# Optimization experiments

Measured on AMD Instinct MI355X. Metric: run time of the kernel, lower is better.

Reference implementation:

```python
import jax, jax.numpy as jnp
import numpy as np
from jax import lax

D, H, W = 50, 50, 50
EPS = 1e-5


def _conv_bn_relu(x, k, gamma, beta, stride):
    # x: (B, Cin, D, H, W), k: (Cout, Cin, 3, 3, 3)
    y = lax.conv_general_dilated(
        x, k, window_strides=(stride, stride, stride),
        padding=[(1, 1), (1, 1), (1, 1)],
        dimension_numbers=("NCDHW", "OIDHW", "NCDHW"))
    # BatchNorm3d in training mode: batch statistics over (N, D, H, W)
    mean = jnp.mean(y, axis=(0, 2, 3, 4), keepdims=True)
    var = jnp.var(y, axis=(0, 2, 3, 4), keepdims=True)
    y = (y - mean) * lax.rsqrt(var + EPS)
    y = y * gamma.reshape(1, -1, 1, 1, 1) + beta.reshape(1, -1, 1, 1, 1)
    return jax.nn.relu(y)


def setup_inputs() -> dict:
    key = jax.random.key(0)
    ks = jax.random.split(key, 16)
    B, N, P, C = 4, 8192, 32, 8
    VD = 128
    s = 0.05
    inp = {
        "voxel_features": jax.random.normal(ks[0], (B, N, P, C), jnp.float32),
        "voxel_coords": jax.random.randint(ks[1], (B, N, 3), 0, 50, jnp.int32),
        "W1": jax.random.normal(ks[2], (C, 64), jnp.float32) * s,
        "b1": jnp.zeros((64,), jnp.float32),
        "W2": jax.random.normal(ks[3], (64, 128), jnp.float32) * s,
        "b2": jnp.zeros((128,), jnp.float32),
        "W3": jax.random.normal(ks[4], (128, VD), jnp.float32) * s,
        "b3": jnp.zeros((VD,), jnp.float32),
        "k1": jax.random.normal(ks[5], (64, VD, 3, 3, 3), jnp.float32) * s,
        "g1": jnp.ones((64,), jnp.float32),
        "be1": jnp.zeros((64,), jnp.float32),
        "k2": jax.random.normal(ks[6], (128, 64, 3, 3, 3), jnp.float32) * s,
        "g2": jnp.ones((128,), jnp.float32),
        "be2": jnp.zeros((128,), jnp.float32),
    }
    return inp


def reference(voxel_features, voxel_coords, W1, b1, W2, b2, W3, b3,
              k1, g1, be1, k2, g2, be2):
    B, N, P, C = voxel_features.shape
    # --- VFE: per-point MLP then max-pool over the P points of each voxel ---
    h = jax.nn.relu(voxel_features @ W1 + b1)      # (B, N, P, 64)
    h = jax.nn.relu(h @ W2 + b2)                   # (B, N, P, 128)
    h = h @ W3 + b3                                # (B, N, P, VD)
    feats = jnp.max(h, axis=2)                     # (B, N, VD)  == MaxPool1d(32)
    VD = feats.shape[-1]
    # --- scatter voxel features into dense grid (replaces B*N python loop) ---
    b_idx = jnp.broadcast_to(jnp.arange(B)[:, None], (B, N))
    vx, vy, vz = voxel_coords[..., 0], voxel_coords[..., 1], voxel_coords[..., 2]
    grid = jnp.zeros((B, D, H, W, VD), feats.dtype)
    grid = grid.at[b_idx, vx, vy, vz].set(feats)   # channel-last scatter
    grid = jnp.transpose(grid, (0, 4, 1, 2, 3))    # (B, VD, D, H, W)
    # --- Conv3d + BN + ReLU stack ---
    y = _conv_bn_relu(grid, k1, g1, be1, stride=1)  # (B, 64, 50, 50, 50)
    y = _conv_bn_relu(y, k2, g2, be2, stride=2)     # (B, 128, 25, 25, 25)
    return y
```

## Files before the change

kernel.cpp:

```cpp
#include <hip/hip_runtime.h>

typedef unsigned short u16;
typedef unsigned int u32;
typedef __attribute__((ext_vector_type(8))) short bf16x8;
typedef __attribute__((ext_vector_type(4))) float f32x4;

#define NB 4
#define NVOX 8192
#define GD 50
#define CELLS 125000

#define OWNER_OFF 0u
#define STATS_OFF 2000000u
#define WT1_OFF   2003072u
#define WT2_OFF   2445440u
#define VW2F_OFF  2887808u
#define VW3F_OFF  2904192u
#define FEATS_OFF 2936960u
#define Y1F_OFF   11325568u

#define S1_SUM 0
#define S1_SQ  64
#define SC1    128
#define SH1    192
#define S2_SUM 256
#define S2_SQ  384
#define SC2    512
#define SH2    640

__device__ __forceinline__ float bf2f(u16 v){ union{u32 u; float f;} x; x.u=((u32)v)<<16; return x.f; }
__device__ __forceinline__ u16 f2bf(float f){ union{u32 u; float f;} x; x.f=f; u32 r = x.u + 0x7fffu + ((x.u>>16)&1u); return (u16)(r>>16); }
__device__ __forceinline__ f32x4 fzero(){ f32x4 v; v[0]=0.f; v[1]=0.f; v[2]=0.f; v[3]=0.f; return v; }

__global__ void k_wt_transform(const float* __restrict__ k1, const float* __restrict__ k2,
                               const float* __restrict__ W2, const float* __restrict__ W3,
                               u16* __restrict__ wt1, u16* __restrict__ wt2,
                               u16* __restrict__ vw2f, u16* __restrict__ vw3f) {
    int idx = blockIdx.x * 256 + threadIdx.x;
    if (idx < 221184) {
        {
            int j = idx & 7, co = (idx>>3)&63, kq = (idx>>9)&3, kc = (idx>>11)&3, s = idx>>13;
            int ci = kc*32 + kq*8 + j;
            wt1[idx] = f2bf(k1[(co*128 + ci)*27 + s]);
        }
        {
            int j = idx & 7, co = (idx>>3)&127, kq = (idx>>10)&3, kc = (idx>>12)&1, s = idx>>13;
            int ci = kc*32 + kq*8 + j;
            wt2[idx] = f2bf(k2[(co*64 + ci)*27 + s]);
        }
    }
    if (idx < 8192) {
        int j = idx & 7, n = (idx>>3)&127, q = idx>>10;
        vw2f[idx] = f2bf(W2[(q*8+j)*128 + n]);
    }
    if (idx < 16384) {
        int j = idx & 7, n = (idx>>3)&127, q = idx>>10;
        vw3f[idx] = f2bf(W3[(q*8+j)*128 + n]);
    }
}

__global__ void k_owner(const int* __restrict__ coords, int* __restrict__ owner) {
    int v = blockIdx.x * 256 + threadIdx.x;
    if (v >= NB*NVOX) return;
    int b = v >> 13, n = v & (NVOX-1);
    int x = coords[v*3], y = coords[v*3+1], z = coords[v*3+2];
    atomicMax(&owner[b*CELLS + (x*GD + y)*GD + z], n);
}

__global__ __launch_bounds__(256, 2) void k_vfe(
        const float* __restrict__ vf,
        const float* __restrict__ W1, const float* __restrict__ b1,
        const float* __restrict__ b2, const float* __restrict__ b3,
        const u16* __restrict__ vw2f, const u16* __restrict__ vw3f,
        u16* __restrict__ feats) {
    const int bid = blockIdx.x;
    const int t = threadIdx.x;
    const int w = t >> 6, lane = t & 63;
    const int lo = lane & 15, hi = lane >> 4;
    const int chgrp = w >> 1, pgrp = w & 1;

    __shared__ __align__(16) char pool[49152];
    u16* h1s = (u16*)pool;
    char* h2s = pool + 16384;
    float* red = (float*)(pool + 16384);

    bf16x8 wa2[2][4], wa3[4][4];
    #pragma unroll
    for (int kk = 0; kk < 2; ++kk)
        #pragma unroll
        for (int cf = 0; cf < 4; ++cf)
            wa2[kk][cf] = *(const bf16x8*)(vw2f + (((kk*4+hi)*128) + chgrp*64 + cf*16 + lo)*8);
    #pragma unroll
    for (int kk = 0; kk < 4; ++kk)
        #pragma unroll
        for (int cf = 0; cf < 4; ++cf)
            wa3[kk][cf] = *(const bf16x8*)(vw3f + (((kk*4+hi)*128) + chgrp*64 + cf*16 + lo)*8);
    f32x4 bb2[4];
    #pragma unroll
    for (int cf = 0; cf < 4; ++cf)
        bb2[cf] = *(const f32x4*)(b2 + chgrp*64 + cf*16 + hi*4);

    {
        const int pt = t & 127, C0 = (t >> 7) * 32;
        f32x4 xv0 = *(const f32x4*)(vf + (size_t)(bid*128 + pt)*8);
        f32x4 xv1 = *(const f32x4*)(vf + (size_t)(bid*128 + pt)*8 + 4);
        float x[8] = {xv0[0],xv0[1],xv0[2],xv0[3],xv1[0],xv1[1],xv1[2],xv1[3]};
        float h[32];
        #pragma unroll
        for (int c = 0; c < 32; ++c) h[c] = b1[C0 + c];
        #pragma unroll
        for (int k = 0; k < 8; ++k) {
            float xk = x[k];
            #pragma unroll
            for (int c = 0; c < 32; ++c) h[c] += xk * W1[k*64 + C0 + c];
        }
        #pragma unroll
        for (int c8 = 0; c8 < 4; ++c8) {
            u16 d8[8];
            #pragma unroll
            for (int j = 0; j < 8; ++j) d8[j] = f2bf(fmaxf(h[c8*8 + j], 0.f));
            int slot = ((C0 >> 3) + c8) ^ (pt & 7);
            *(uint4*)(h1s + pt*64 + slot*8) = *(uint4*)d8;
        }
    }
    __syncthreads();

    f32x4 acc2[4][4];
    #pragma unroll
    for (int cf = 0; cf < 4; ++cf)
        #pragma unroll
        for (int pf = 0; pf < 4; ++pf) acc2[cf][pf] = fzero();
    #pragma unroll
    for (int kk = 0; kk < 2; ++kk) {
        bf16x8 bh[4];
        #pragma unroll
        for (int pf = 0; pf < 4; ++pf) {
            int pt = pgrp*64 + pf*16 + lo;
            bh[pf] = *(const bf16x8*)(h1s + pt*64 + (((kk*4+hi) ^ (pt&7)) << 3));
        }
        #pragma unroll
        for (int cf = 0; cf < 4; ++cf)
            #pragma unroll
            for (int pf = 0; pf < 4; ++pf)
                acc2[cf][pf] = __builtin_amdgcn_mfma_f32_16x16x32_bf16(wa2[kk][cf], bh[pf], acc2[cf][pf], 0, 0, 0);
    }
    #pragma unroll
    for (int cf = 0; cf < 4; ++cf) {
        #pragma unroll
        for (int pf = 0; pf < 4; ++pf) {
            int pt = pgrp*64 + pf*16 + lo;
            float v0 = fmaxf(acc2[cf][pf][0] + bb2[cf][0], 0.f);
            float v1 = fmaxf(acc2[cf][pf][1] + bb2[cf][1], 0.f);
            float v2 = fmaxf(acc2[cf][pf][2] + bb2[cf][2], 0.f);
            float v3 = fmaxf(acc2[cf][pf][3] + bb2[cf][3], 0.f);
            uint2 d;
            d.x = (u32)f2bf(v0) | ((u32)f2bf(v1) << 16);
            d.y = (u32)f2bf(v2) | ((u32)f2bf(v3) << 16);
            int s = (chgrp*8 + cf*2 + (hi>>1)) ^ (pt & 15);
            *(uint2*)(h2s + pt*256 + s*16 + (hi&1)*8) = d;
        }
    }
    __syncthreads();

    f32x4 acc3[4][4];
    #pragma unroll
    for (int cf = 0; cf < 4; ++cf)
        #pragma unroll
        for (int pf = 0; pf < 4; ++pf) acc3[cf][pf] = fzero();
    #pragma unroll
    for (int kk = 0; kk < 4; ++kk) {
        bf16x8 bh[4];
        #pragma unroll
        for (int pf = 0; pf < 4; ++pf) {
            int pt = pgrp*64 + pf*16 + lo;
            bh[pf] = *(const bf16x8*)(h2s + pt*256 + (((kk*4+hi) ^ (pt&15)) << 4));
        }
        #pragma unroll
        for (int cf = 0; cf < 4; ++cf)
            #pragma unroll
            for (int pf = 0; pf < 4; ++pf)
                acc3[cf][pf] = __builtin_amdgcn_mfma_f32_16x16x32_bf16(wa3[kk][cf], bh[pf], acc3[cf][pf], 0, 0, 0);
    }
    __syncthreads();

    #pragma unroll
    for (int vox01 = 0; vox01 < 2; ++vox01) {
        int vv = pgrp*2 + vox01;
        #pragma unroll
        for (int cf = 0; cf < 4; ++cf) {
            f32x4 mx;
            #pragma unroll
            for (int r = 0; r < 4; ++r)
                mx[r] = fmaxf(acc3[cf][vox01*2][r], acc3[cf][vox01*2+1][r]);
            int s4 = (cf*4 + hi) ^ lo;
            *(f32x4*)(red + vv*2048 + lo*128 + chgrp*64 + s4*4) = mx;
        }
    }
    __syncthreads();

    #pragma unroll
    for (int half = 0; half < 2; ++half) {
        int vv = (t >> 7) + half*2;
        int ch = t & 127;
        int cq = (ch & 63) >> 2, e = ch & 3, cg = ch >> 6;
        float m = -3.0e38f;
        #pragma unroll
        for (int lo2 = 0; lo2 < 16; ++lo2)
            m = fmaxf(m, red[vv*2048 + lo2*128 + cg*64 + ((cq ^ lo2) << 2) + e]);
        int gv = bid*4 + vv;
        feats[(size_t)gv*128 + ch] = f2bf(m + b3[ch]);
    }
}

__global__ __launch_bounds__(256, 3) void k_conv1t(
        const u16* __restrict__ feats, const int* __restrict__ owner,
        const u16* __restrict__ wt1, float* __restrict__ y1f,
        float* __restrict__ stats) {
    const int tx = blockIdx.x, ty = blockIdx.y;
    const int b = blockIdx.z >> 1, h = blockIdx.z & 1;
    const int z0 = h*25;
    const int t = threadIdx.x;
    const int w = t >> 6, lane = t & 63;
    const int lo = lane & 15, hi = lane >> 4;

    __shared__ __align__(16) float acc[4*100*20];
    __shared__ int list[432];
    __shared__ int cnt;

    if (t == 0) cnt = 0;
    for (int i = t; i < 2000; i += 256)
        *(f32x4*)(acc + i*4) = fzero();
    __syncthreads();

    for (int i = t; i < 432; i += 256) {
        int hxr = i / 108, r2 = i - hxr*108;
        int hyr = r2 / 27, zz = r2 - hyr*27;
        int z = z0 - 1 + zz;
        int hx = 2*tx - 1 + hxr, hy = 2*ty - 1 + hyr;
        if (hx >= 0 && hx < GD && hy >= 0 && hy < GD && z >= 0 && z < GD) {
            int n = owner[b*CELLS + (hx*GD + hy)*GD + z];
            if (n >= 0) {
                int idx = atomicAdd(&cnt, 1);
                list[idx] = n | (hxr << 13) | (hyr << 15) | (z << 17);
            }
        }
    }
    __syncthreads();
    const int C = cnt;
    float* accw = acc + w*2000;

    for (int g = 0; g*32 < C; ++g) {
        int e0 = 0, e1 = 0; bool v0 = false, v1 = false;
        { int i0 = g*32 + lo;      if (i0 < C) { e0 = list[i0]; v0 = true; } }
        { int i1 = g*32 + 16 + lo; if (i1 < C) { e1 = list[i1]; v1 = true; } }
        const u16* f0 = feats + (size_t)(b*NVOX + (e0 & 8191))*128 + hi*8;
        const u16* f1 = feats + (size_t)(b*NVOX + (e1 & 8191))*128 + hi*8;
        bf16x8 bb0[4], bb1[4];
        #pragma unroll
        for (int kc = 0; kc < 4; ++kc) bb0[kc] = *(const bf16x8*)(f0 + kc*32);
        #pragma unroll
        for (int kc = 0; kc < 4; ++kc) bb1[kc] = *(const bf16x8*)(f1 + kc*32);
        const int hx0 = (e0>>13)&3, hy0 = (e0>>15)&3, zz0 = (e0>>17)&63;
        const int hx1 = (e1>>13)&3, hy1 = (e1>>15)&3, zz1 = (e1>>17)&63;
        const bool two = (g*32 + 16 < C);

        #pragma unroll 1
        for (int s = 0; s < 27; ++s) {
            const int dx = s/9, r9 = s - dx*9, dy = r9/3, dz = r9 - dy*3;
            bf16x8 a[4];
            #pragma unroll
            for (int kc = 0; kc < 4; ++kc)
                a[kc] = *(const bf16x8*)(wt1 + (size_t)((s*4 + kc)*4 + hi)*512 + (w*16 + lo)*8);
            {
                int oxr = hx0 - dx, oyr = hy0 - dy, ozl = zz0 + 1 - dz - z0;
                bool val = v0 && ((unsigned)oxr < 2u) && ((unsigned)oyr < 2u)
                              && ((unsigned)ozl < 25u);
                f32x4 d = fzero();
                #pragma unroll
                for (int kc = 0; kc < 4; ++kc)
                    d = __builtin_amdgcn_mfma_f32_16x16x32_bf16(a[kc], bb0[kc], d, 0, 0, 0);
                if (val) {
                    float* p = accw + ((oxr*2 + oyr)*25 + ozl)*20 + hi*4;
                    f32x4 o = *(f32x4*)p;
                    o[0] += d[0]; o[1] += d[1]; o[2] += d[2]; o[3] += d[3];
                    *(f32x4*)p = o;
                }
            }
            if (two) {
                int oxr = hx1 - dx, oyr = hy1 - dy, ozl = zz1 + 1 - dz - z0;
                bool val = v1 && ((unsigned)oxr < 2u) && ((unsigned)oyr < 2u)
                              && ((unsigned)ozl < 25u);
                f32x4 d = fzero();
                #pragma unroll
                for (int kc = 0; kc < 4; ++kc)
                    d = __builtin_amdgcn_mfma_f32_16x16x32_bf16(a[kc], bb1[kc], d, 0, 0, 0);
                if (val) {
                    float* p = accw + ((oxr*2 + oyr)*25 + ozl)*20 + hi*4;
                    f32x4 o = *(f32x4*)p;
                    o[0] += d[0]; o[1] += d[1]; o[2] += d[2]; o[3] += d[3];
                    *(f32x4*)p = o;
                }
            }
        }
    }
    __syncthreads();

    float s4[4] = {0.f,0.f,0.f,0.f}, q4[4] = {0.f,0.f,0.f,0.f};
    const int cq = t & 15;
    for (int i = t; i < 1600; i += 256) {
        int cell = i >> 4;
        f32x4 v = *(const f32x4*)(acc + (cq>>2)*2000 + cell*20 + (cq&3)*4);
        int col = cell / 25, ozl = cell - col*25;
        int ox = 2*tx + (col >> 1), oy = 2*ty + (col & 1);
        *(f32x4*)(y1f + (size_t)((b*GD + ox)*GD + oy)*3200 + (z0 + ozl)*64 + cq*4) = v;
        #pragma unroll
        for (int e2 = 0; e2 < 4; ++e2) { s4[e2] += v[e2]; q4[e2] += v[e2]*v[e2]; }
    }
    __syncthreads();
    #pragma unroll
    for (int e2 = 0; e2 < 4; ++e2) {
        acc[t*8 + e2]     = s4[e2];
        acc[t*8 + 4 + e2] = q4[e2];
    }
    __syncthreads();
    if (t < 128) {
        int isq = t >> 6, ch = t & 63, cq0 = ch >> 2, e2 = ch & 3;
        float sum = 0.f;
        #pragma unroll
        for (int k = 0; k < 16; ++k)
            sum += acc[(cq0 + 16*k)*8 + isq*4 + e2];
        atomicAdd(&stats[(isq ? S1_SQ : S1_SUM) + ch], sum);
    }
}

__global__ void k_finalize(float* __restrict__ stats, const float* __restrict__ g,
                           const float* __restrict__ be, int C, float cnt,
                           int st_off, int sc_off, int sh_off) {
    int t = threadIdx.x;
    if (t < C) {
        float mean = stats[st_off + t] / cnt;
        float var  = stats[st_off + C + t] / cnt - mean*mean;
        float inv  = rsqrtf(var + 1e-5f);
        stats[sc_off + t] = g[t]*inv;
        stats[sh_off + t] = be[t] - mean*g[t]*inv;
    }
}

__global__ __launch_bounds__(256, 4) void k_conv2(
        const float* __restrict__ y1f, const u16* __restrict__ wt2,
        float* __restrict__ stats, float* __restrict__ out) {
    const int ox = blockIdx.x, oyp = blockIdx.y, b = blockIdx.z;
    const int t = threadIdx.x;
    const int w = t >> 6, lane = t & 63;
    const int col = w >> 1, nh = w & 1, lo = lane & 15, hi = lane >> 4;

    __shared__ __align__(16) char pool[26624];
    u16* in2 = (u16*)pool;
    float* red2 = (float*)(pool + 25600);
    red2[t] = 0.f;

    const float* sc1 = stats + SC1;
    const float* sh1 = stats + SH1;

    f32x4 acc[2][4];
    #pragma unroll
    for (int m=0;m<2;m++){ acc[m][0]=fzero(); acc[m][1]=fzero(); acc[m][2]=fzero(); acc[m][3]=fzero(); }

    const int oy = 2*oyp + col;
    for (int dxy = 0; dxy < 9; ++dxy) {
        int dx = dxy/3, dy = dxy - dx*3;
        int xi = 2*ox + dx - 1;
        bool okx = (xi >= 0) && (xi < GD);
        __syncthreads();
        for (int i = t; i < 832; i += 256) {
            int c = (i >= 416) ? 1 : 0;
            int cc = i - c*416;
            int z = cc >> 3, sl = cc & 7;
            int oyc = 2*oyp + c;
            int yi = 2*oyc + dy - 1;
            bool ok = okx && (oyc < 25) && (yi >= 0) && (yi < GD) && (z >= 1) && (z <= 50);
            u16 d8[8];
            if (ok) {
                const float* src = y1f + (size_t)((b*GD + xi)*GD + yi)*3200 + cc*8 - 64;
                f32x4 v0 = *(const f32x4*)src;
                f32x4 v1 = *(const f32x4*)(src + 4);
                #pragma unroll
                for (int j=0;j<4;j++) {
                    int ci = sl*8 + j;
                    d8[j] = f2bf(fmaxf(v0[j]*sc1[ci] + sh1[ci], 0.f));
                }
                #pragma unroll
                for (int j=0;j<4;j++) {
                    int ci = sl*8 + 4 + j;
                    d8[4+j] = f2bf(fmaxf(v1[j]*sc1[ci] + sh1[ci], 0.f));
                }
            } else {
                #pragma unroll
                for (int j=0;j<8;j++) d8[j] = 0;
            }
            *(uint4*)(in2 + (c*52 + z)*64 + ((sl ^ ((z>>1) & 7)) << 3)) = *(uint4*)d8;
        }
        __syncthreads();
        const u16* wsrc = wt2 + dxy*24576;
        #pragma unroll
        for (int dz = 0; dz < 3; ++dz) {
            #pragma unroll
            for (int kc = 0; kc < 2; ++kc) {
                bf16x8 a[2], bbw[4];
                #pragma unroll
                for (int mf = 0; mf < 2; ++mf) {
                    int z = 2*(mf*16 + lo) + dz; z = (z > 51) ? 51 : z;
                    a[mf] = *(const bf16x8*)(in2 + (col*52 + z)*64 + (((kc*4 + hi) ^ ((z>>1) & 7)) << 3));
                }
                #pragma unroll
                for (int nf = 0; nf < 4; ++nf)
                    bbw[nf] = *(const bf16x8*)(wsrc + (((dz*2 + kc)*4 + hi)*128 + (nh*4 + nf)*16 + lo)*8);
                #pragma unroll
                for (int mf = 0; mf < 2; ++mf) {
                    #pragma unroll
                    for (int nf = 0; nf < 4; ++nf)
                        acc[mf][nf] = __builtin_amdgcn_mfma_f32_16x16x32_bf16(a[mf], bbw[nf], acc[mf][nf], 0, 0, 0);
                }
            }
        }
    }
    __syncthreads();
    float* trans = (float*)pool;
    if (oy < 25) {
        #pragma unroll
        for (int nf = 0; nf < 4; ++nf) {
            float s = 0.f, q = 0.f;
            int co = (nh*4 + nf)*16 + lo;
            #pragma unroll
            for (int mf = 0; mf < 2; ++mf) {
                #pragma unroll
                for (int r = 0; r < 4; ++r) {
                    int o = mf*16 + hi*4 + r;
                    if (o < 25) {
                        float vv = acc[mf][nf][r];
                        trans[(col*128 + co)*25 + o] = vv;
                        s += vv; q += vv*vv;
                    }
                }
            }
            atomicAdd(&red2[co], s);
            atomicAdd(&red2[128 + co], q);
        }
    }
    __syncthreads();
    if (t < 128) {
        atomicAdd(&stats[S2_SUM + t], red2[t]);
        atomicAdd(&stats[S2_SQ  + t], red2[128 + t]);
    }
    for (int i = t; i < 6400; i += 256) {
        int c = i / 3200; int r = i - c*3200;
        int co = r / 25;  int oz = r - co*25;
        int oyc = 2*oyp + c;
        if (oyc < 25)
            out[((size_t)(b*128 + co)*625 + ox*25 + oyc)*25 + oz] = trans[(c*128 + co)*25 + oz];
    }
}

__global__ void k_bnrelu2(float* __restrict__ out, const float* __restrict__ stats) {
    int idx = blockIdx.x*256 + threadIdx.x;
    if (idx >= 8000000) return;
    int co = (idx / 15625) & 127;
    float v = out[idx];
    out[idx] = fmaxf(v*stats[SC2 + co] + stats[SH2 + co], 0.f);
}

extern "C" void kernel_launch(void* const* d_in, const int* in_sizes, int n_in,
                              void* d_out, int out_size, void* d_ws, size_t ws_size,
                              hipStream_t stream) {
    const float* vf     = (const float*)d_in[0];
    const int*   coords = (const int*)  d_in[1];
    const float* W1 = (const float*)d_in[2];
    const float* b1 = (const float*)d_in[3];
    const float* W2 = (const float*)d_in[4];
    const float* b2 = (const float*)d_in[5];
    const float* W3 = (const float*)d_in[6];
    const float* b3 = (const float*)d_in[7];
    const float* k1 = (const float*)d_in[8];
    const float* g1 = (const float*)d_in[9];
    const float* be1= (const float*)d_in[10];
    const float* k2 = (const float*)d_in[11];
    const float* g2 = (const float*)d_in[12];
    const float* be2= (const float*)d_in[13];

    char* ws = (char*)d_ws;
    int*   owner = (int*)  (ws + OWNER_OFF);
    float* stats = (float*)(ws + STATS_OFF);
    u16*   wt1   = (u16*)  (ws + WT1_OFF);
    u16*   wt2   = (u16*)  (ws + WT2_OFF);
    u16*   vw2f  = (u16*)  (ws + VW2F_OFF);
    u16*   vw3f  = (u16*)  (ws + VW3F_OFF);
    u16*   feats = (u16*)  (ws + FEATS_OFF);
    float* y1f   = (float*)(ws + Y1F_OFF);
    float* out   = (float*)d_out;

    hipMemsetAsync(owner, 0xFF, (size_t)NB*CELLS*4, stream);
    hipMemsetAsync(stats, 0, 768*4, stream);

    k_wt_transform<<<864, 256, 0, stream>>>(k1, k2, W2, W3, wt1, wt2, vw2f, vw3f);
    k_owner<<<(NB*NVOX+255)/256, 256, 0, stream>>>(coords, owner);
    k_vfe<<<NB*NVOX/4, 256, 0, stream>>>(vf, W1, b1, b2, b3, vw2f, vw3f, feats);
    k_conv1t<<<dim3(25,25,NB*2), 256, 0, stream>>>(feats, owner, wt1, y1f, stats);
    k_finalize<<<1, 64, 0, stream>>>(stats, g1, be1, 64, 500000.f, S1_SUM, SC1, SH1);
    k_conv2<<<dim3(25,13,NB), 256, 0, stream>>>(y1f, wt2, stats, out);
    k_finalize<<<1, 128, 0, stream>>>(stats, g2, be2, 128, 62500.f, S2_SUM, SC2, SH2);
    k_bnrelu2<<<(8000000+255)/256, 256, 0, stream>>>(out, stats);
}
```

Baseline: 425.9 us.

## Restructure conv1 tap loop, defer VFE weight loads, raise occupancy, grid-stride BN

In k_vfe, the layer-3 weight fragments are now loaded after the layer-2 stage instead of at kernel start, which shortens register live ranges, and launch bounds rise to 3 blocks per CU. In k_conv1t, each group now takes 16 voxels instead of two halves of 32, and the 27-tap loop becomes 9 xy-taps that each issue the three z-taps together, giving more independent MFMAs per weight-load batch; launch bounds rise to 4. The final BN+ReLU kernel becomes a grid-stride loop over 2048 blocks. Higher occupancy targets may force register spills, and the conv1 change loads more weight registers at once.

```diff
diff --git a/kernel.cpp b/kernel.cpp
--- a/kernel.cpp
+++ b/kernel.cpp
@@ -67,7 +67,7 @@
     atomicMax(&owner[b*CELLS + (x*GD + y)*GD + z], n);
 }
 
-__global__ __launch_bounds__(256, 2) void k_vfe(
+__global__ __launch_bounds__(256, 3) void k_vfe(
         const float* __restrict__ vf,
         const float* __restrict__ W1, const float* __restrict__ b1,
         const float* __restrict__ b2, const float* __restrict__ b3,
@@ -84,17 +84,12 @@
     char* h2s = pool + 16384;
     float* red = (float*)(pool + 16384);
 
-    bf16x8 wa2[2][4], wa3[4][4];
+    bf16x8 wa2[2][4];
     #pragma unroll
     for (int kk = 0; kk < 2; ++kk)
         #pragma unroll
         for (int cf = 0; cf < 4; ++cf)
             wa2[kk][cf] = *(const bf16x8*)(vw2f + (((kk*4+hi)*128) + chgrp*64 + cf*16 + lo)*8);
-    #pragma unroll
-    for (int kk = 0; kk < 4; ++kk)
-        #pragma unroll
-        for (int cf = 0; cf < 4; ++cf)
-            wa3[kk][cf] = *(const bf16x8*)(vw3f + (((kk*4+hi)*128) + chgrp*64 + cf*16 + lo)*8);
     f32x4 bb2[4];
     #pragma unroll
     for (int cf = 0; cf < 4; ++cf)
@@ -162,6 +157,13 @@
     }
     __syncthreads();
 
+    bf16x8 wa3[4][4];
+    #pragma unroll
+    for (int kk = 0; kk < 4; ++kk)
+        #pragma unroll
+        for (int cf = 0; cf < 4; ++cf)
+            wa3[kk][cf] = *(const bf16x8*)(vw3f + (((kk*4+hi)*128) + chgrp*64 + cf*16 + lo)*8);
+
     f32x4 acc3[4][4];
     #pragma unroll
     for (int cf = 0; cf < 4; ++cf)
@@ -212,7 +214,7 @@
     }
 }
 
-__global__ __launch_bounds__(256, 3) void k_conv1t(
+__global__ __launch_bounds__(256, 4) void k_conv1t(
         const u16* __restrict__ feats, const int* __restrict__ owner,
         const u16* __restrict__ wt1, float* __restrict__ y1f,
         float* __restrict__ stats) {
@@ -249,58 +251,60 @@
     const int C = cnt;
     float* accw = acc + w*2000;
 
-    for (int g = 0; g*32 < C; ++g) {
-        int e0 = 0, e1 = 0; bool v0 = false, v1 = false;
-        { int i0 = g*32 + lo;      if (i0 < C) { e0 = list[i0]; v0 = true; } }
-        { int i1 = g*32 + 16 + lo; if (i1 < C) { e1 = list[i1]; v1 = true; } }
-        const u16* f0 = feats + (size_t)(b*NVOX + (e0 & 8191))*128 + hi*8;
-        const u16* f1 = feats + (size_t)(b*NVOX + (e1 & 8191))*128 + hi*8;
-        bf16x8 bb0[4], bb1[4];
-        #pragma unroll
-        for (int kc = 0; kc < 4; ++kc) bb0[kc] = *(const bf16x8*)(f0 + kc*32);
-        #pragma unroll
-        for (int kc = 0; kc < 4; ++kc) bb1[kc] = *(const bf16x8*)(f1 + kc*32);
-        const int hx0 = (e0>>13)&3, hy0 = (e0>>15)&3, zz0 = (e0>>17)&63;
-        const int hx1 = (e1>>13)&3, hy1 = (e1>>15)&3, zz1 = (e1>>17)&63;
-        const bool two = (g*32 + 16 < C);
+    const int ngrp = (C + 15) >> 4;
+    for (int g = 0; g < ngrp; ++g) {
+        int ii = g*16 + lo;
+        int e = 0; bool v = false;
+        if (ii < C) { e = list[ii]; v = true; }
+        const int n = e & 8191;
+        const u16* fsrc = feats + (size_t)(b*NVOX + n)*128 + hi*8;
+        bf16x8 bb[4];
+        #pragma unroll
+        for (int kc = 0; kc < 4; ++kc) bb[kc] = *(const bf16x8*)(fsrc + kc*32);
+        const int hxr = (e>>13)&3, hyr = (e>>15)&3, zv = (e>>17)&63;
+        const int ozb = zv + 1 - z0;
 
         #pragma unroll 1
-        for (int s = 0; s < 27; ++s) {
-            const int dx = s/9, r9 = s - dx*9, dy = r9/3, dz = r9 - dy*3;
-            bf16x8 a[4];
-            #pragma unroll
-            for (int kc = 0; kc < 4; ++kc)
-                a[kc] = *(const bf16x8*)(wt1 + (size_t)((s*4 + kc)*4 + hi)*512 + (w*16 + lo)*8);
-            {
-                int oxr = hx0 - dx, oyr = hy0 - dy, ozl = zz0 + 1 - dz - z0;
-                bool val = v0 && ((unsigned)oxr < 2u) && ((unsigned)oyr < 2u)
-                              && ((unsigned)ozl < 25u);
-                f32x4 d = fzero();
-                #pragma unroll
-                for (int kc = 0; kc < 4; ++kc)
-                    d = __builtin_amdgcn_mfma_f32_16x16x32_bf16(a[kc], bb0[kc], d, 0, 0, 0);
-                if (val) {
-                    float* p = accw + ((oxr*2 + oyr)*25 + ozl)*20 + hi*4;
-                    f32x4 o = *(f32x4*)p;
-                    o[0] += d[0]; o[1] += d[1]; o[2] += d[2]; o[3] += d[3];
-                    *(f32x4*)p = o;
-                }
-            }
-            if (two) {
-                int oxr = hx1 - dx, oyr = hy1 - dy, ozl = zz1 + 1 - dz - z0;
-                bool val = v1 && ((unsigned)oxr < 2u) && ((unsigned)oyr < 2u)
-                              && ((unsigned)ozl < 25u);
-                f32x4 d = fzero();
-                #pragma unroll
-                for (int kc = 0; kc < 4; ++kc)
-                    d = __builtin_amdgcn_mfma_f32_16x16x32_bf16(a[kc], bb1[kc], d, 0, 0, 0);
-                if (val) {
-                    float* p = accw + ((oxr*2 + oyr)*25 + ozl)*20 + hi*4;
-                    f32x4 o = *(f32x4*)p;
-                    o[0] += d[0]; o[1] += d[1]; o[2] += d[2]; o[3] += d[3];
-                    *(f32x4*)p = o;
-                }
-            }
+        for (int dxy = 0; dxy < 9; ++dxy) {
+            const int dx = dxy/3, dy = dxy - dx*3;
+            const int oxr = hxr - dx, oyr = hyr - dy;
+            const bool vxy = v && ((unsigned)oxr < 2u) && ((unsigned)oyr < 2u);
+            bf16x8 a0[4], a1[4], a2[4];
+            #pragma unroll
+            for (int kc = 0; kc < 4; ++kc) {
+                a0[kc] = *(const bf16x8*)(wt1 + (size_t)(((dxy*3+0)*4 + kc)*4 + hi)*512 + (w*16 + lo)*8);
+                a1[kc] = *(const bf16x8*)(wt1 + (size_t)(((dxy*3+1)*4 + kc)*4 + hi)*512 + (w*16 + lo)*8);
+                a2[kc] = *(const bf16x8*)(wt1 + (size_t)(((dxy*3+2)*4 + kc)*4 + hi)*512 + (w*16 + lo)*8);
+            }
+            f32x4 d0 = fzero(), d1 = fzero(), d2 = fzero();
+            #pragma unroll
+            for (int kc = 0; kc < 4; ++kc) {
+                d0 = __builtin_amdgcn_mfma_f32_16x16x32_bf16(a0[kc], bb[kc], d0, 0, 0, 0);
+                d1 = __builtin_amdgcn_mfma_f32_16x16x32_bf16(a1[kc], bb[kc], d1, 0, 0, 0);
+                d2 = __builtin_amdgcn_mfma_f32_16x16x32_bf16(a2[kc], bb[kc], d2, 0, 0, 0);
+            }
+            const int cb = (oxr*2 + oyr)*25;
+            if (vxy && (unsigned)ozb < 25u) {
+                float* p = accw + (cb + ozb)*20 + hi*4;
+                f32x4 o = *(f32x4*)p;
+                o[0]+=d0[0]; o[1]+=d0[1]; o[2]+=d0[2]; o[3]+=d0[3];
+                *(f32x4*)p = o;
+            }
+            asm volatile("" ::: "memory");
+            if (vxy && (unsigned)(ozb-1) < 25u) {
+                float* p = accw + (cb + ozb-1)*20 + hi*4;
+                f32x4 o = *(f32x4*)p;
+                o[0]+=d1[0]; o[1]+=d1[1]; o[2]+=d1[2]; o[3]+=d1[3];
+                *(f32x4*)p = o;
+            }
+            asm volatile("" ::: "memory");
+            if (vxy && (unsigned)(ozb-2) < 25u) {
+                float* p = accw + (cb + ozb-2)*20 + hi*4;
+                f32x4 o = *(f32x4*)p;
+                o[0]+=d2[0]; o[1]+=d2[1]; o[2]+=d2[2]; o[3]+=d2[3];
+                *(f32x4*)p = o;
+            }
+            asm volatile("" ::: "memory");
         }
     }
     __syncthreads();
@@ -462,11 +466,11 @@
 }
 
 __global__ void k_bnrelu2(float* __restrict__ out, const float* __restrict__ stats) {
-    int idx = blockIdx.x*256 + threadIdx.x;
-    if (idx >= 8000000) return;
-    int co = (idx / 15625) & 127;
-    float v = out[idx];
-    out[idx] = fmaxf(v*stats[SC2 + co] + stats[SH2 + co], 0.f);
+    for (int idx = blockIdx.x*256 + threadIdx.x; idx < 8000000; idx += 2048*256) {
+        int co = (idx / 15625) & 127;
+        float v = out[idx];
+        out[idx] = fmaxf(v*stats[SC2 + co] + stats[SH2 + co], 0.f);
+    }
 }
 
 extern "C" void kernel_launch(void* const* d_in, const int* in_sizes, int n_in,
@@ -508,5 +512,5 @@
     k_finalize<<<1, 64, 0, stream>>>(stats, g1, be1, 64, 500000.f, S1_SUM, SC1, SH1);
     k_conv2<<<dim3(25,13,NB), 256, 0, stream>>>(y1f, wt2, stats, out);
     k_finalize<<<1, 128, 0, stream>>>(stats, g2, be2, 128, 62500.f, S2_SUM, SC2, SH2);
-    k_bnrelu2<<<(8000000+255)/256, 256, 0, stream>>>(out, stats);
-}
+    k_bnrelu2<<<2048, 256, 0, stream>>>(out, stats);
+}
```

Result: slower. 448.5 us, median of 2 (+5.3%).
